# Kernel tuning notes

Measured on AMD Instinct MI355X. Metric: run time of the kernel, lower is better.

Reference implementation:

```python
import jax, jax.numpy as jnp
import numpy as np

N_NODES = 100000
N_EDGES = 1600000
N_MOVES = 200000
D = 256          # in_channels
H = 512          # hidden_dim

def setup_inputs() -> dict:
    key = jax.random.key(0)
    ks = jax.random.split(key, 6)
    node_embeddings = jax.random.normal(ks[0], (N_NODES, D), dtype=jnp.float32)
    edge_index = jax.random.randint(ks[1], (2, N_EDGES), 0, N_NODES, dtype=jnp.int64)
    move_edge_idxs = jax.random.randint(ks[2], (N_MOVES,), 0, N_EDGES, dtype=jnp.int64)
    # torch Linear weights: [out, in], scaled like kaiming-uniform-ish
    W1 = jax.random.normal(ks[3], (H, 2 * D), dtype=jnp.float32) * (1.0 / np.sqrt(2 * D))
    b1 = jnp.zeros((H,), dtype=jnp.float32)
    W2 = jax.random.normal(ks[4], (H // 2, H), dtype=jnp.float32) * (1.0 / np.sqrt(H))
    b2 = jnp.zeros((H // 2,), dtype=jnp.float32)
    W3 = jax.random.normal(ks[5], (1, H // 2), dtype=jnp.float32) * (1.0 / np.sqrt(H // 2))
    b3 = jnp.zeros((1,), dtype=jnp.float32)
    return {"node_embeddings": node_embeddings, "edge_index": edge_index,
            "move_edge_idxs": move_edge_idxs, "W1": W1, "b1": b1,
            "W2": W2, "b2": b2, "W3": W3, "b3": b3}

def reference(node_embeddings, edge_index, move_edge_idxs, W1, b1, W2, b2, W3, b3):
    # candidate_moves = edge_index[:, move_edge_idxs].T -> [n_moves, 2]
    src = edge_index[0, move_edge_idxs]          # [n_moves]
    tgt = edge_index[1, move_edge_idxs]          # [n_moves]
    emb_src = node_embeddings[src]               # [n_moves, D]
    emb_tgt = node_embeddings[tgt]               # [n_moves, D]
    x = jnp.concatenate([emb_src, emb_tgt], axis=-1)   # [n_moves, 2D]
    # 3-layer MLP (dropout is identity in eval mode)
    h = jax.nn.relu(x @ W1.T + b1)               # [n_moves, H]
    h = jax.nn.relu(h @ W2.T + b2)               # [n_moves, H//2]
    logits = (h @ W3.T + b3).squeeze(-1)         # [n_moves]
    return logits
```

## Files before the change

### kernel.cpp

```cpp
#include <hip/hip_runtime.h>
#include <hip/hip_bf16.h>

typedef __attribute__((ext_vector_type(4))) float f32x4;
typedef __attribute__((ext_vector_type(8))) short bfrag;
typedef __attribute__((ext_vector_type(4))) float facc;
typedef __attribute__((ext_vector_type(8))) ushort u16x8;

#define N_MOVES 200000
#define N_EDGES 1600000
#define DEMB 256
#define KD 512
#define H1D 512
#define H2D 256
#define MT 64
#define NTHREADS 512

__device__ __forceinline__ ushort f2b(float f) {
  union { float f; unsigned u; } x; x.f = f;
  unsigned r = (x.u + 0x7fffu + ((x.u >> 16) & 1u)) >> 16;
  return (ushort)r;
}
__device__ __forceinline__ float b2f(ushort h) {
  union { unsigned u; float f; } x; x.u = ((unsigned)h) << 16;
  return x.f;
}

__global__ void convert_w(const float* __restrict__ W1, const float* __restrict__ W2,
                          ushort* __restrict__ Wb) {
  int i = (blockIdx.x * 256 + threadIdx.x) * 4;
  const int n1 = H1D * KD;
  if (i < n1) {
    f32x4 v = *(const f32x4*)(W1 + i);
    ushort4 h = { f2b(v.x), f2b(v.y), f2b(v.z), f2b(v.w) };
    *(ushort4*)(Wb + i) = h;
  } else {
    int j = i - n1;
    f32x4 v = *(const f32x4*)(W2 + j);
    ushort4 h = { f2b(v.x), f2b(v.y), f2b(v.z), f2b(v.w) };
    *(ushort4*)(Wb + n1 + j) = h;
  }
}

__global__ void convert_emb(const float* __restrict__ E, ushort* __restrict__ Eb) {
  int i = (blockIdx.x * 256 + threadIdx.x) * 8;
  f32x4 a = *(const f32x4*)(E + i);
  f32x4 b = *(const f32x4*)(E + i + 4);
  u16x8 h = { f2b(a.x), f2b(a.y), f2b(a.z), f2b(a.w),
              f2b(b.x), f2b(b.y), f2b(b.z), f2b(b.w) };
  *(u16x8*)(Eb + i) = h;
}

template<int EMBBF>
__global__ __launch_bounds__(NTHREADS, 4)
void fused_mlp(const float* __restrict__ emb,
               const ushort* __restrict__ embb,
               const int* __restrict__ edge_index,
               const int* __restrict__ move_idx,
               const ushort* __restrict__ W1b,
               const float* __restrict__ b1,
               const ushort* __restrict__ W2b,
               const float* __restrict__ b2,
               const float* __restrict__ W3,
               const float* __restrict__ b3,
               float* __restrict__ out)
{
  __shared__ ushort bufA[MT][KD];
  __shared__ int   s_src[MT], s_tgt[MT];
  __shared__ float sW3[H2D];

  const int tid  = threadIdx.x;
  const int lane = tid & 63;
  const int wave = tid >> 6;
  const int m0   = blockIdx.x * MT;

  if (tid < MT) {
    int e = move_idx[m0 + tid];
    s_src[tid] = edge_index[e];
    s_tgt[tid] = edge_index[N_EDGES + e];
  }
  if (tid < H2D) sW3[tid] = W3[tid];
  __syncthreads();

  const int arow = lane & 15;
  const int akE  = (lane >> 4) << 3;
  const int akB  = (lane >> 4) << 4;

  const ushort* wp0 = W1b + (size_t)(((wave << 6) + arow) * KD) + akE;
  const ushort* wp1 = wp0 + 16 * KD;
  const ushort* wp2 = wp0 + 32 * KD;
  const ushort* wp3 = wp0 + 48 * KD;

  bfrag bA[4], bB[4];
  bA[0] = *(const bfrag*)(wp0);      bA[1] = *(const bfrag*)(wp1);
  bA[2] = *(const bfrag*)(wp2);      bA[3] = *(const bfrag*)(wp3);
  bB[0] = *(const bfrag*)(wp0 + 32); bB[1] = *(const bfrag*)(wp1 + 32);
  bB[2] = *(const bfrag*)(wp2 + 32); bB[3] = *(const bfrag*)(wp3 + 32);

  if (EMBBF) {
    #pragma unroll
    for (int it = 0; it < 8; ++it) {
      int row  = (wave << 3) + it;
      int gl   = lane ^ (row & 7);
      int node = (gl < 32) ? s_src[row] : s_tgt[row];
      const ushort* gp = embb + (size_t)node * DEMB + ((size_t)(gl & 31) << 3);
      __builtin_amdgcn_global_load_lds(
          (const __attribute__((address_space(1))) void*)gp,
          (__attribute__((address_space(3))) void*)(&bufA[row][0]),
          16, 0, 0);
    }
  } else {
    for (int u = tid; u < MT * 128; u += NTHREADS) {
      int row = u >> 7;
      int c4  = u & 127;
      const float* sp = (c4 < 64) ? (emb + (size_t)s_src[row] * DEMB + (c4 << 2))
                                  : (emb + (size_t)s_tgt[row] * DEMB + ((c4 - 64) << 2));
      f32x4 v = *(const f32x4*)sp;
      ushort4 h = { f2b(v.x), f2b(v.y), f2b(v.z), f2b(v.w) };
      int bo = (c4 << 3) ^ ((row & 7) << 4);
      *(ushort4*)((char*)(&bufA[row][0]) + bo) = h;
    }
  }
  __syncthreads();

  facc acc[4][4] = {};
  #pragma unroll
  for (int kk2 = 0; kk2 < 8; ++kk2) {
    const int kk = kk2 << 1;
    __builtin_amdgcn_s_setprio(1);
    #pragma unroll
    for (int mg = 0; mg < 4; ++mg) {
      int row = (mg << 4) + arow;
      int bo = ((kk << 6) + akB) ^ ((row & 7) << 4);
      bfrag a = *(const bfrag*)((const char*)(&bufA[row][0]) + bo);
      #pragma unroll
      for (int ng = 0; ng < 4; ++ng)
        acc[mg][ng] = __builtin_amdgcn_mfma_f32_16x16x32_bf16(a, bA[ng], acc[mg][ng], 0, 0, 0);
    }
    __builtin_amdgcn_s_setprio(0);
    if (kk + 2 < 16) {
      bA[0] = *(const bfrag*)(wp0 + ((kk + 2) << 5));
      bA[1] = *(const bfrag*)(wp1 + ((kk + 2) << 5));
      bA[2] = *(const bfrag*)(wp2 + ((kk + 2) << 5));
      bA[3] = *(const bfrag*)(wp3 + ((kk + 2) << 5));
    }
    __builtin_amdgcn_s_setprio(1);
    #pragma unroll
    for (int mg = 0; mg < 4; ++mg) {
      int row = (mg << 4) + arow;
      int bo = (((kk + 1) << 6) + akB) ^ ((row & 7) << 4);
      bfrag a = *(const bfrag*)((const char*)(&bufA[row][0]) + bo);
      #pragma unroll
      for (int ng = 0; ng < 4; ++ng)
        acc[mg][ng] = __builtin_amdgcn_mfma_f32_16x16x32_bf16(a, bB[ng], acc[mg][ng], 0, 0, 0);
    }
    __builtin_amdgcn_s_setprio(0);
    if (kk + 3 < 16) {
      bB[0] = *(const bfrag*)(wp0 + ((kk + 3) << 5));
      bB[1] = *(const bfrag*)(wp1 + ((kk + 3) << 5));
      bB[2] = *(const bfrag*)(wp2 + ((kk + 3) << 5));
      bB[3] = *(const bfrag*)(wp3 + ((kk + 3) << 5));
    }
  }

  const ushort* cp0 = W2b + (size_t)(((wave << 5) + arow) * KD) + akE;
  const ushort* cp1 = cp0 + 16 * KD;
  bfrag cA[2], cB[2];
  cA[0] = *(const bfrag*)(cp0);      cA[1] = *(const bfrag*)(cp1);
  cB[0] = *(const bfrag*)(cp0 + 32); cB[1] = *(const bfrag*)(cp1 + 32);

  float bias1[4];
  #pragma unroll
  for (int ng = 0; ng < 4; ++ng) bias1[ng] = b1[(wave << 6) + (ng << 4) + arow];

  __syncthreads();

  #pragma unroll
  for (int ng = 0; ng < 4; ++ng) {
    int col = (wave << 6) + (ng << 4) + arow;
    #pragma unroll
    for (int mg = 0; mg < 4; ++mg) {
      #pragma unroll
      for (int r = 0; r < 4; ++r) {
        int row = (mg << 4) + ((lane >> 4) << 2) + r;
        float v = fmaxf(acc[mg][ng][r] + bias1[ng], 0.f);
        int bo = (col << 1) ^ ((row & 7) << 4);
        *(ushort*)((char*)(&bufA[row][0]) + bo) = f2b(v);
      }
    }
  }
  __syncthreads();

  facc acc2[4][2] = {};
  #pragma unroll
  for (int kk2 = 0; kk2 < 8; ++kk2) {
    const int kk = kk2 << 1;
    __builtin_amdgcn_s_setprio(1);
    #pragma unroll
    for (int mg = 0; mg < 4; ++mg) {
      int row = (mg << 4) + arow;
      int bo = ((kk << 6) + akB) ^ ((row & 7) << 4);
      bfrag a = *(const bfrag*)((const char*)(&bufA[row][0]) + bo);
      #pragma unroll
      for (int ng = 0; ng < 2; ++ng)
        acc2[mg][ng] = __builtin_amdgcn_mfma_f32_16x16x32_bf16(a, cA[ng], acc2[mg][ng], 0, 0, 0);
    }
    __builtin_amdgcn_s_setprio(0);
    if (kk + 2 < 16) {
      cA[0] = *(const bfrag*)(cp0 + ((kk + 2) << 5));
      cA[1] = *(const bfrag*)(cp1 + ((kk + 2) << 5));
    }
    __builtin_amdgcn_s_setprio(1);
    #pragma unroll
    for (int mg = 0; mg < 4; ++mg) {
      int row = (mg << 4) + arow;
      int bo = (((kk + 1) << 6) + akB) ^ ((row & 7) << 4);
      bfrag a = *(const bfrag*)((const char*)(&bufA[row][0]) + bo);
      #pragma unroll
      for (int ng = 0; ng < 2; ++ng)
        acc2[mg][ng] = __builtin_amdgcn_mfma_f32_16x16x32_bf16(a, cB[ng], acc2[mg][ng], 0, 0, 0);
    }
    __builtin_amdgcn_s_setprio(0);
    if (kk + 3 < 16) {
      cB[0] = *(const bfrag*)(cp0 + ((kk + 3) << 5));
      cB[1] = *(const bfrag*)(cp1 + ((kk + 3) << 5));
    }
  }

  float bias2[2];
  #pragma unroll
  for (int ng = 0; ng < 2; ++ng) bias2[ng] = b2[(wave << 5) + (ng << 4) + arow];

  __syncthreads();

  ushort (*H2s)[H2D] = (ushort(*)[H2D])bufA;
  #pragma unroll
  for (int ng = 0; ng < 2; ++ng) {
    int col = (wave << 5) + (ng << 4) + arow;
    #pragma unroll
    for (int mg = 0; mg < 4; ++mg) {
      #pragma unroll
      for (int r = 0; r < 4; ++r) {
        int row = (mg << 4) + ((lane >> 4) << 2) + r;
        float v = fmaxf(acc2[mg][ng][r] + bias2[ng], 0.f);
        int bo = (col << 1) ^ ((row & 7) << 4);
        *(ushort*)((char*)(&H2s[row][0]) + bo) = f2b(v);
      }
    }
  }
  __syncthreads();

  {
    const float b3v = b3[0];
    int row = tid >> 3;
    int oct = tid & 7;
    float sum = 0.f;
    #pragma unroll
    for (int j = 0; j < 4; ++j) {
      int kb = (oct << 6) + (j << 4);
      int bo = kb ^ ((row & 7) << 4);
      bfrag hv = *(const bfrag*)((const char*)(&H2s[row][0]) + bo);
      int k0 = (oct << 5) + (j << 3);
      #pragma unroll
      for (int e = 0; e < 8; ++e)
        sum += b2f((ushort)hv[e]) * sW3[k0 + e];
    }
    sum += __shfl_xor(sum, 1);
    sum += __shfl_xor(sum, 2);
    sum += __shfl_xor(sum, 4);
    if (oct == 0) out[m0 + row] = sum + b3v;
  }
}

extern "C" void kernel_launch(void* const* d_in, const int* in_sizes, int n_in,
                              void* d_out, int out_size, void* d_ws, size_t ws_size,
                              hipStream_t stream) {
  const float* emb        = (const float*)d_in[0];
  const int*   edge_index = (const int*)d_in[1];
  const int*   move_idx   = (const int*)d_in[2];
  const float* W1         = (const float*)d_in[3];
  const float* b1         = (const float*)d_in[4];
  const float* W2         = (const float*)d_in[5];
  const float* b2         = (const float*)d_in[6];
  const float* W3         = (const float*)d_in[7];
  const float* b3         = (const float*)d_in[8];
  float* out = (float*)d_out;

  ushort* Wb   = (ushort*)d_ws;
  ushort* Embb = Wb + (H1D * KD + H2D * KD);
  const size_t need = (size_t)(H1D * KD + H2D * KD + 100000 * DEMB) * 2;

  convert_w<<<384, 256, 0, stream>>>(W1, W2, Wb);

  if (ws_size >= need) {
    convert_emb<<<12500, 256, 0, stream>>>(emb, Embb);
    fused_mlp<1><<<N_MOVES / MT, NTHREADS, 0, stream>>>(
        emb, Embb, edge_index, move_idx,
        Wb, b1, Wb + H1D * KD, b2, W3, b3, out);
  } else {
    fused_mlp<0><<<N_MOVES / MT, NTHREADS, 0, stream>>>(
        emb, Embb, edge_index, move_idx,
        Wb, b1, Wb + H1D * KD, b2, W3, b3, out);
  }
}
```

Measured before the change: 480.9 us.

## Double-buffer LDS activations, swap MFMA operands, prefetch A fragments

Adds a second 64x512 bf16 LDS buffer so layer-1 output goes to bufB without a barrier to finish reading bufA. MFMA operands are swapped so each lane holds 4 consecutive output columns, which allows vectorized ushort4 stores and folding the bias into the accumulator init. LDS A-fragments are now prefetched one k-step ahead into registers. Together this removes two __syncthreads and the scalar 16-bit stores. The cost is doubled shared memory, with launch bounds lowered from 4 to 2 blocks per CU, which reduces occupancy.

```diff
diff --git a/kernel.cpp b/kernel.cpp
--- a/kernel.cpp
+++ b/kernel.cpp
@@ -51,7 +51,7 @@
 }
 
 template<int EMBBF>
-__global__ __launch_bounds__(NTHREADS, 4)
+__global__ __launch_bounds__(NTHREADS, 2)
 void fused_mlp(const float* __restrict__ emb,
                const ushort* __restrict__ embb,
                const int* __restrict__ edge_index,
@@ -65,6 +65,7 @@
                float* __restrict__ out)
 {
   __shared__ ushort bufA[MT][KD];
+  __shared__ ushort bufB[MT][KD];
   __shared__ int   s_src[MT], s_tgt[MT];
   __shared__ float sW3[H2D];
 
@@ -84,6 +85,7 @@
   const int arow = lane & 15;
   const int akE  = (lane >> 4) << 3;
   const int akB  = (lane >> 4) << 4;
+  const int nq   = (lane >> 4) << 2;
 
   const ushort* wp0 = W1b + (size_t)(((wave << 6) + arow) * KD) + akE;
   const ushort* wp1 = wp0 + 16 * KD;
@@ -122,37 +124,58 @@
   }
   __syncthreads();
 
-  facc acc[4][4] = {};
+  facc acc[4][4];
+  #pragma unroll
+  for (int ng = 0; ng < 4; ++ng) {
+    f32x4 bv = *(const f32x4*)(b1 + (wave << 6) + (ng << 4) + nq);
+    #pragma unroll
+    for (int mg = 0; mg < 4; ++mg) acc[mg][ng] = bv;
+  }
+
+  bfrag aE[4], aO[4];
+  #pragma unroll
+  for (int mg = 0; mg < 4; ++mg) {
+    int row = (mg << 4) + arow;
+    int bo = akB ^ ((row & 7) << 4);
+    aE[mg] = *(const bfrag*)((const char*)(&bufA[row][0]) + bo);
+  }
+
   #pragma unroll
   for (int kk2 = 0; kk2 < 8; ++kk2) {
     const int kk = kk2 << 1;
+    if (kk + 1 < 16) {
+      #pragma unroll
+      for (int mg = 0; mg < 4; ++mg) {
+        int row = (mg << 4) + arow;
+        int bo = (((kk + 1) << 6) + akB) ^ ((row & 7) << 4);
+        aO[mg] = *(const bfrag*)((const char*)(&bufA[row][0]) + bo);
+      }
+    }
     __builtin_amdgcn_s_setprio(1);
     #pragma unroll
-    for (int mg = 0; mg < 4; ++mg) {
-      int row = (mg << 4) + arow;
-      int bo = ((kk << 6) + akB) ^ ((row & 7) << 4);
-      bfrag a = *(const bfrag*)((const char*)(&bufA[row][0]) + bo);
+    for (int mg = 0; mg < 4; ++mg)
       #pragma unroll
       for (int ng = 0; ng < 4; ++ng)
-        acc[mg][ng] = __builtin_amdgcn_mfma_f32_16x16x32_bf16(a, bA[ng], acc[mg][ng], 0, 0, 0);
-    }
+        acc[mg][ng] = __builtin_amdgcn_mfma_f32_16x16x32_bf16(bA[ng], aE[mg], acc[mg][ng], 0, 0, 0);
     __builtin_amdgcn_s_setprio(0);
     if (kk + 2 < 16) {
       bA[0] = *(const bfrag*)(wp0 + ((kk + 2) << 5));
       bA[1] = *(const bfrag*)(wp1 + ((kk + 2) << 5));
       bA[2] = *(const bfrag*)(wp2 + ((kk + 2) << 5));
       bA[3] = *(const bfrag*)(wp3 + ((kk + 2) << 5));
+      #pragma unroll
+      for (int mg = 0; mg < 4; ++mg) {
+        int row = (mg << 4) + arow;
+        int bo = (((kk + 2) << 6) + akB) ^ ((row & 7) << 4);
+        aE[mg] = *(const bfrag*)((const char*)(&bufA[row][0]) + bo);
+      }
     }
     __builtin_amdgcn_s_setprio(1);
     #pragma unroll
-    for (int mg = 0; mg < 4; ++mg) {
-      int row = (mg << 4) + arow;
-      int bo = (((kk + 1) << 6) + akB) ^ ((row & 7) << 4);
-      bfrag a = *(const bfrag*)((const char*)(&bufA[row][0]) + bo);
+    for (int mg = 0; mg < 4; ++mg)
       #pragma unroll
       for (int ng = 0; ng < 4; ++ng)
-        acc[mg][ng] = __builtin_amdgcn_mfma_f32_16x16x32_bf16(a, bB[ng], acc[mg][ng], 0, 0, 0);
-    }
+        acc[mg][ng] = __builtin_amdgcn_mfma_f32_16x16x32_bf16(bB[ng], aO[mg], acc[mg][ng], 0, 0, 0);
     __builtin_amdgcn_s_setprio(0);
     if (kk + 3 < 16) {
       bB[0] = *(const bfrag*)(wp0 + ((kk + 3) << 5));
@@ -168,57 +191,72 @@
   cA[0] = *(const bfrag*)(cp0);      cA[1] = *(const bfrag*)(cp1);
   cB[0] = *(const bfrag*)(cp0 + 32); cB[1] = *(const bfrag*)(cp1 + 32);
 
-  float bias1[4];
-  #pragma unroll
-  for (int ng = 0; ng < 4; ++ng) bias1[ng] = b1[(wave << 6) + (ng << 4) + arow];
-
+  #pragma unroll
+  for (int mg = 0; mg < 4; ++mg) {
+    int m = (mg << 4) + arow;
+    #pragma unroll
+    for (int ng = 0; ng < 4; ++ng) {
+      int nb = (wave << 6) + (ng << 4) + nq;
+      ushort4 h;
+      h.x = f2b(fmaxf(acc[mg][ng][0], 0.f));
+      h.y = f2b(fmaxf(acc[mg][ng][1], 0.f));
+      h.z = f2b(fmaxf(acc[mg][ng][2], 0.f));
+      h.w = f2b(fmaxf(acc[mg][ng][3], 0.f));
+      int bo = (nb << 1) ^ ((m & 7) << 4);
+      *(ushort4*)((char*)(&bufB[0][0]) + m * (KD * 2) + bo) = h;
+    }
+  }
   __syncthreads();
 
-  #pragma unroll
-  for (int ng = 0; ng < 4; ++ng) {
-    int col = (wave << 6) + (ng << 4) + arow;
-    #pragma unroll
-    for (int mg = 0; mg < 4; ++mg) {
-      #pragma unroll
-      for (int r = 0; r < 4; ++r) {
-        int row = (mg << 4) + ((lane >> 4) << 2) + r;
-        float v = fmaxf(acc[mg][ng][r] + bias1[ng], 0.f);
-        int bo = (col << 1) ^ ((row & 7) << 4);
-        *(ushort*)((char*)(&bufA[row][0]) + bo) = f2b(v);
-      }
-    }
-  }
-  __syncthreads();
-
-  facc acc2[4][2] = {};
+  facc acc2[4][2];
+  #pragma unroll
+  for (int ng = 0; ng < 2; ++ng) {
+    f32x4 bv = *(const f32x4*)(b2 + (wave << 5) + (ng << 4) + nq);
+    #pragma unroll
+    for (int mg = 0; mg < 4; ++mg) acc2[mg][ng] = bv;
+  }
+
+  #pragma unroll
+  for (int mg = 0; mg < 4; ++mg) {
+    int row = (mg << 4) + arow;
+    int bo = akB ^ ((row & 7) << 4);
+    aE[mg] = *(const bfrag*)((const char*)(&bufB[row][0]) + bo);
+  }
+
   #pragma unroll
   for (int kk2 = 0; kk2 < 8; ++kk2) {
     const int kk = kk2 << 1;
+    if (kk + 1 < 16) {
+      #pragma unroll
+      for (int mg = 0; mg < 4; ++mg) {
+        int row = (mg << 4) + arow;
+        int bo = (((kk + 1) << 6) + akB) ^ ((row & 7) << 4);
+        aO[mg] = *(const bfrag*)((const char*)(&bufB[row][0]) + bo);
+      }
+    }
     __builtin_amdgcn_s_setprio(1);
     #pragma unroll
-    for (int mg = 0; mg < 4; ++mg) {
-      int row = (mg << 4) + arow;
-      int bo = ((kk << 6) + akB) ^ ((row & 7) << 4);
-      bfrag a = *(const bfrag*)((const char*)(&bufA[row][0]) + bo);
+    for (int mg = 0; mg < 4; ++mg)
       #pragma unroll
       for (int ng = 0; ng < 2; ++ng)
-        acc2[mg][ng] = __builtin_amdgcn_mfma_f32_16x16x32_bf16(a, cA[ng], acc2[mg][ng], 0, 0, 0);
-    }
+        acc2[mg][ng] = __builtin_amdgcn_mfma_f32_16x16x32_bf16(cA[ng], aE[mg], acc2[mg][ng], 0, 0, 0);
     __builtin_amdgcn_s_setprio(0);
     if (kk + 2 < 16) {
       cA[0] = *(const bfrag*)(cp0 + ((kk + 2) << 5));
       cA[1] = *(const bfrag*)(cp1 + ((kk + 2) << 5));
+      #pragma unroll
+      for (int mg = 0; mg < 4; ++mg) {
+        int row = (mg << 4) + arow;
+        int bo = (((kk + 2) << 6) + akB) ^ ((row & 7) << 4);
+        aE[mg] = *(const bfrag*)((const char*)(&bufB[row][0]) + bo);
+      }
     }
     __builtin_amdgcn_s_setprio(1);
     #pragma unroll
-    for (int mg = 0; mg < 4; ++mg) {
-      int row = (mg << 4) + arow;
-      int bo = (((kk + 1) << 6) + akB) ^ ((row & 7) << 4);
-      bfrag a = *(const bfrag*)((const char*)(&bufA[row][0]) + bo);
+    for (int mg = 0; mg < 4; ++mg)
       #pragma unroll
       for (int ng = 0; ng < 2; ++ng)
-        acc2[mg][ng] = __builtin_amdgcn_mfma_f32_16x16x32_bf16(a, cB[ng], acc2[mg][ng], 0, 0, 0);
-    }
+        acc2[mg][ng] = __builtin_amdgcn_mfma_f32_16x16x32_bf16(cB[ng], aO[mg], acc2[mg][ng], 0, 0, 0);
     __builtin_amdgcn_s_setprio(0);
     if (kk + 3 < 16) {
       cB[0] = *(const bfrag*)(cp0 + ((kk + 3) << 5));
@@ -226,25 +264,20 @@
     }
   }
 
-  float bias2[2];
-  #pragma unroll
-  for (int ng = 0; ng < 2; ++ng) bias2[ng] = b2[(wave << 5) + (ng << 4) + arow];
-
-  __syncthreads();
-
   ushort (*H2s)[H2D] = (ushort(*)[H2D])bufA;
   #pragma unroll
-  for (int ng = 0; ng < 2; ++ng) {
-    int col = (wave << 5) + (ng << 4) + arow;
-    #pragma unroll
-    for (int mg = 0; mg < 4; ++mg) {
-      #pragma unroll
-      for (int r = 0; r < 4; ++r) {
-        int row = (mg << 4) + ((lane >> 4) << 2) + r;
-        float v = fmaxf(acc2[mg][ng][r] + bias2[ng], 0.f);
-        int bo = (col << 1) ^ ((row & 7) << 4);
-        *(ushort*)((char*)(&H2s[row][0]) + bo) = f2b(v);
-      }
+  for (int mg = 0; mg < 4; ++mg) {
+    int m = (mg << 4) + arow;
+    #pragma unroll
+    for (int ng = 0; ng < 2; ++ng) {
+      int nb = (wave << 5) + (ng << 4) + nq;
+      ushort4 h;
+      h.x = f2b(fmaxf(acc2[mg][ng][0], 0.f));
+      h.y = f2b(fmaxf(acc2[mg][ng][1], 0.f));
+      h.z = f2b(fmaxf(acc2[mg][ng][2], 0.f));
+      h.w = f2b(fmaxf(acc2[mg][ng][3], 0.f));
+      int bo = (nb << 1) ^ ((m & 7) << 4);
+      *(ushort4*)((char*)(&H2s[0][0]) + m * (H2D * 2) + bo) = h;
     }
   }
   __syncthreads();
```

Measured after the change: 524.7 us. 1.09x slower.
